# Kernel optimization log

Measured on AMD Instinct MI355X. Metric: run time of the kernel, lower is better.

## Reference

```python
import jax, jax.numpy as jnp
import numpy as np

B, T, I = 64, 1024, 256
H1, H2, O = 512, 512, 128


def setup_inputs() -> dict:
    key = jax.random.key(0)
    ks = jax.random.split(key, 4)
    x = jax.random.normal(ks[0], (B, T, I), dtype=jnp.float32)
    W1 = jax.random.normal(ks[1], (H1, I), dtype=jnp.float32) / np.sqrt(I).astype(np.float32)
    b1 = jnp.zeros((H1,), jnp.float32)
    tau_m1 = jnp.full((H1,), 2.0, jnp.float32)
    tau_n1 = jnp.full((H1,), 2.0, jnp.float32)
    W2 = jax.random.normal(ks[2], (H2, H1), dtype=jnp.float32) / np.sqrt(H1).astype(np.float32)
    b2 = jnp.zeros((H2,), jnp.float32)
    tau_m2 = jnp.full((H2,), 2.0, jnp.float32)
    tau_n2 = jnp.full((H2,), 2.0, jnp.float32)
    Wo = jax.random.normal(ks[3], (O, H2), dtype=jnp.float32) / np.sqrt(H2).astype(np.float32)
    bo = jnp.zeros((O,), jnp.float32)
    return {"x": x, "W1": W1, "b1": b1, "tau_m1": tau_m1, "tau_n1": tau_n1,
            "W2": W2, "b2": b2, "tau_m2": tau_m2, "tau_n2": tau_n2,
            "Wo": Wo, "bo": bo}


def reference(x, W1, b1, tau_m1, tau_n1, W2, b2, tau_m2, tau_n2, Wo, bo):
    dt = x.dtype
    beta1 = jax.nn.sigmoid(tau_n1)   # input-decay layer 1
    alpha1 = jax.nn.sigmoid(tau_m1)  # membrane-decay layer 1
    beta2 = jax.nn.sigmoid(tau_n2)
    alpha2 = jax.nn.sigmoid(tau_m2)

    # layer-1 dense projection is time-independent of state -> batch it: [T,B,H1]
    d_in1_all = jnp.swapaxes(jnp.einsum('bti,hi->bth', x, W1) + b1, 0, 1)

    def step(carry, d_in1):
        mem1, d1, mem2, d2 = carry
        # layer 1: dual-decay LIF
        d1 = beta1 * d1 + (1.0 - beta1) * d_in1
        mem1 = alpha1 * mem1 + (1.0 - alpha1) * d1
        s1 = (mem1 > 1.0).astype(dt)
        mem1 = mem1 * (1.0 - s1)
        # layer 2
        d_in2 = s1 @ W2.T + b2
        d2 = beta2 * d2 + (1.0 - beta2) * d_in2
        mem2 = alpha2 * mem2 + (1.0 - alpha2) * d2
        s2 = (mem2 > 1.0).astype(dt)
        mem2 = mem2 * (1.0 - s2)
        out = jax.nn.sigmoid(s2 @ Wo.T + bo)
        return (mem1, d1, mem2, d2), out

    init = (jnp.zeros((B, H1), dt), jnp.zeros((B, H1), dt),
            jnp.zeros((B, H2), dt), jnp.zeros((B, H2), dt))
    _, outs = jax.lax.scan(step, init, d_in1_all)  # [T,B,O]
    return jnp.swapaxes(outs, 0, 1)  # [B,T,O]
```

## Files before the change

### kernel.cpp

```cpp
#include <hip/hip_runtime.h>
#include <hip/hip_bf16.h>
#include <cstdint>

#define B_  64
#define T_  1024
#define I_  256
#define H1_ 512
#define H2_ 512
#define O_  128
#define CH_ 16
#define LL_ 64
#define GUARD_ 1e-3f

typedef unsigned long long u64;
typedef __attribute__((ext_vector_type(8))) short s8v;
typedef __attribute__((ext_vector_type(4))) float f4v;

__device__ __forceinline__ unsigned short f2bf(float f) {
    unsigned int u = __float_as_uint(f);
    unsigned int r = (u + 0x7FFFu + ((u >> 16) & 1u)) >> 16;
    return (unsigned short)r;
}

__global__ __launch_bounds__(256) void prep_kernel(
    const float* __restrict__ W2, const float* __restrict__ Wo,
    const float* __restrict__ W1,
    float* __restrict__ W2T, float* __restrict__ WoT,
    unsigned short* __restrict__ W1b,
    u64* __restrict__ zbuf, int nwords)
{
    int idx = blockIdx.x * 256 + threadIdx.x;
    if (idx < H1_ * H2_) {
        int h1 = idx / H2_, h2 = idx % H2_;
        W2T[idx] = W2[h2 * H1_ + h1];
    }
    if (idx < H2_ * O_) {
        int h2 = idx / O_, o = idx % O_;
        WoT[idx] = Wo[o * H2_ + h2];
    }
    if (idx < H1_ * I_) {
        W1b[idx] = f2bf(W1[idx]);
    }
    for (int i = idx; i < nwords; i += 256 * 1024)
        zbuf[i] = 0ull;
}

__global__ __launch_bounds__(1024, 1) void fused1_kernel(
    const float* __restrict__ X,
    const unsigned short* __restrict__ W1b,
    const float* __restrict__ b1,
    const float* __restrict__ tau_m1, const float* __restrict__ tau_n1,
    u64* __restrict__ s1_bits, u64* __restrict__ s1_any)
{
    __shared__ float rbuf[CH_][64][16];
    __shared__ float vd[CH_][64];
    __shared__ float meS[CH_][64];
    __shared__ float thS[CH_][64];
    __shared__ float memio[64];
    __shared__ int hdirty[64];
    __shared__ int anyd;

    const int tid = threadIdx.x;
    const int h  = tid & 63;
    const int c  = tid >> 6;
    const int id = blockIdx.x;
    const int b  = id & 63;
    const int hg = id >> 6;
    const int n0 = hg * 64;
    const int lr = tid & 15;
    const int lq = (tid >> 4) & 3;

    if (tid < 64) hdirty[tid] = 0;
    if (tid == 0) anyd = 0;

    f4v acc[4][4] = {};
    const float* xb = X + ((size_t)b * T_ + c * LL_) * I_;
    #pragma unroll
    for (int ks = 0; ks < 8; ks++) {
        s8v bf[4];
        #pragma unroll
        for (int ni = 0; ni < 4; ni++)
            bf[ni] = *reinterpret_cast<const s8v*>(
                W1b + (size_t)(n0 + ni * 16 + lr) * I_ + ks * 32 + lq * 8);
        #pragma unroll
        for (int mi = 0; mi < 4; mi++) {
            const float* xp = xb + (size_t)(mi * 16 + lr) * I_ + ks * 32 + lq * 8;
            float4 v0 = *reinterpret_cast<const float4*>(xp);
            float4 v1 = *reinterpret_cast<const float4*>(xp + 4);
            s8v a;
            a[0] = (short)((__float_as_uint(v0.x) + 0x8000u) >> 16);
            a[1] = (short)((__float_as_uint(v0.y) + 0x8000u) >> 16);
            a[2] = (short)((__float_as_uint(v0.z) + 0x8000u) >> 16);
            a[3] = (short)((__float_as_uint(v0.w) + 0x8000u) >> 16);
            a[4] = (short)((__float_as_uint(v1.x) + 0x8000u) >> 16);
            a[5] = (short)((__float_as_uint(v1.y) + 0x8000u) >> 16);
            a[6] = (short)((__float_as_uint(v1.z) + 0x8000u) >> 16);
            a[7] = (short)((__float_as_uint(v1.w) + 0x8000u) >> 16);
            #pragma unroll
            for (int ni = 0; ni < 4; ni++)
                acc[mi][ni] = __builtin_amdgcn_mfma_f32_16x16x32_bf16(
                    a, bf[ni], acc[mi][ni], 0, 0, 0);
        }
    }

    const float biasv = b1[n0 + h];
    const int swz_w = (lr & 3) ^ (lr >> 2);
    const int swz_r = (h & 3) ^ ((h >> 2) & 3);
    float arr[LL_];
    #pragma unroll
    for (int mi = 0; mi < 4; mi++) {
        #pragma unroll
        for (int ni = 0; ni < 4; ni++) {
            *reinterpret_cast<float4*>(&rbuf[c][ni * 16 + lr][(lq ^ swz_w) * 4]) =
                make_float4(acc[mi][ni][0], acc[mi][ni][1],
                            acc[mi][ni][2], acc[mi][ni][3]);
        }
        __builtin_amdgcn_wave_barrier();
        #pragma unroll
        for (int jq = 0; jq < 4; jq++) {
            float4 rv = *reinterpret_cast<const float4*>(&rbuf[c][h][(jq ^ swz_r) * 4]);
            arr[mi * 16 + jq * 4 + 0] = rv.x + biasv;
            arr[mi * 16 + jq * 4 + 1] = rv.y + biasv;
            arr[mi * 16 + jq * 4 + 2] = rv.z + biasv;
            arr[mi * 16 + jq * 4 + 3] = rv.w + biasv;
        }
        __builtin_amdgcn_wave_barrier();
    }

    const int hglob = n0 + h;
    float beta    = 1.f / (1.f + __expf(-tau_n1[hglob]));
    float alpha   = 1.f / (1.f + __expf(-tau_m1[hglob]));
    float ombeta  = 1.f - beta;
    float omalpha = 1.f - alpha;
    float bL = beta;  { bL *= bL; bL *= bL; bL *= bL; bL *= bL; bL *= bL; bL *= bL; }
    float aL = alpha; { aL *= aL; aL *= aL; aL *= aL; aL *= aL; aL *= aL; aL *= aL; }
    float ai = 1.0f / alpha;

    float d1 = 0.f;
    #pragma unroll
    for (int i = 0; i < LL_; i++) {
        d1 = fmaf(beta, d1, ombeta * arr[i]);
        arr[i] = d1;
    }
    vd[c][h] = d1;
    __syncthreads();

    float ds = 0.f;
    for (int cc = 0; cc < c; cc++) ds = fmaf(bL, ds, vd[cc][h]);

    float pc = ds, m = 0.f, api = 1.f, th = 3.4e38f;
    #pragma unroll
    for (int i = 0; i < LL_; i++) {
        pc *= beta;
        float dt = arr[i] + pc;
        arr[i] = dt;
        m = fmaf(alpha, m, omalpha * dt);
        api *= ai;
        th = fminf(th, (1.f - m) * api);
    }
    meS[c][h] = m;
    thS[c][h] = th;
    __syncthreads();

    float v = 0.f; bool dirty = false;
    for (int cc = 0; cc < c; cc++) {
        if (v > thS[cc][h] - GUARD_) dirty = true;
        v = fmaf(aL, v, meS[cc][h]);
    }
    if (v > th - GUARD_) dirty = true;
    if (dirty) { hdirty[h] = 1; atomicOr(&anyd, 1); }
    __syncthreads();

    if (anyd) {
        for (int cc = 0; cc < CH_; cc++) {
            if (c == cc && hdirty[h]) {
                float mi_ = (cc == 0) ? 0.f : memio[h];
                float mo;
                if (mi_ > th - GUARD_) {
                    float mem = mi_;
                    #pragma unroll
                    for (int i = 0; i < LL_; i++) {
                        mem = fmaf(alpha, mem, omalpha * arr[i]);
                        if (mem > 1.f) {
                            atomicOr(&s1_bits[((size_t)b * T_ + cc * LL_ + i) * 8 + hg], 1ull << h);
                            atomicOr(&s1_any[b * 16 + cc], 1ull << i);
                            mem = 0.f;
                        }
                    }
                    mo = mem;
                } else {
                    mo = fmaf(aL, mi_, m);
                }
                memio[h] = mo;
            }
            __syncthreads();
        }
    }
}

__device__ __noinline__ float gather_w2(const u64* __restrict__ w,
                                        const float* __restrict__ W2T, int hglob)
{
    float acc = 0.f;
    for (int q = 0; q < 8; q++) {
        u64 mq = w[q];
        while (mq) {
            int h1 = __ffsll((long long)mq) - 1;
            mq &= mq - 1;
            acc += W2T[(size_t)(q * 64 + h1) * H2_ + hglob];
        }
    }
    return acc;
}

__global__ __launch_bounds__(1024) void scan2_kernel(
    const float* __restrict__ W2T, const float* __restrict__ b2,
    const float* __restrict__ tau_m2, const float* __restrict__ tau_n2,
    const u64* __restrict__ s1_bits, const u64* __restrict__ s1_any,
    u64* __restrict__ s2_bits, u64* __restrict__ s2_any)
{
    __shared__ float vd[CH_][64];
    __shared__ float meS[CH_][64];
    __shared__ float thS[CH_][64];
    __shared__ float memio[64];
    __shared__ int hdirty[64];
    __shared__ int anyd;

    int tid = threadIdx.x;
    int h = tid & 63, c = tid >> 6;
    int id = blockIdx.x;
    int b  = id & 63;
    int hg = id >> 6;
    int hglob = hg * 64 + h;

    if (tid < 64) hdirty[tid] = 0;
    if (tid == 0) anyd = 0;

    float beta    = 1.f / (1.f + __expf(-tau_n2[hglob]));
    float alpha   = 1.f / (1.f + __expf(-tau_m2[hglob]));
    float ombeta  = 1.f - beta;
    float omalpha = 1.f - alpha;
    float bias    = b2[hglob];
    float bL = beta;  { bL *= bL; bL *= bL; bL *= bL; bL *= bL; bL *= bL; bL *= bL; }
    float aL = alpha; { aL *= aL; aL *= aL; aL *= aL; aL *= aL; aL *= aL; aL *= aL; }
    float ai = 1.0f / alpha;

    float arr[LL_];
    u64 aw = s1_any[b * 16 + c];
    float d2 = 0.f;
    if (aw == 0) {
        #pragma unroll
        for (int i = 0; i < LL_; i++) {
            d2 = fmaf(beta, d2, ombeta * bias);
            arr[i] = d2;
        }
    } else {
        #pragma unroll
        for (int i = 0; i < LL_; i++) {
            float dv = bias;
            if ((aw >> i) & 1ull)
                dv += gather_w2(s1_bits + ((size_t)b * T_ + c * LL_ + i) * 8, W2T, hglob);
            d2 = fmaf(beta, d2, ombeta * dv);
            arr[i] = d2;
        }
    }
    vd[c][h] = d2;
    __syncthreads();

    float ds = 0.f;
    for (int cc = 0; cc < c; cc++) ds = fmaf(bL, ds, vd[cc][h]);

    float pc = ds, m = 0.f, api = 1.f, th = 3.4e38f;
    #pragma unroll
    for (int i = 0; i < LL_; i++) {
        pc *= beta;
        float dt = arr[i] + pc;
        arr[i] = dt;
        m = fmaf(alpha, m, omalpha * dt);
        api *= ai;
        th = fminf(th, (1.f - m) * api);
    }
    meS[c][h] = m;
    thS[c][h] = th;
    __syncthreads();

    float v = 0.f; bool dirty = false;
    for (int cc = 0; cc < c; cc++) {
        if (v > thS[cc][h] - GUARD_) dirty = true;
        v = fmaf(aL, v, meS[cc][h]);
    }
    if (v > th - GUARD_) dirty = true;
    if (dirty) { hdirty[h] = 1; atomicOr(&anyd, 1); }
    __syncthreads();

    if (anyd) {
        for (int cc = 0; cc < CH_; cc++) {
            if (c == cc && hdirty[h]) {
                float mi_ = (cc == 0) ? 0.f : memio[h];
                float mo;
                if (mi_ > th - GUARD_) {
                    float mem = mi_;
                    #pragma unroll
                    for (int i = 0; i < LL_; i++) {
                        mem = fmaf(alpha, mem, omalpha * arr[i]);
                        if (mem > 1.f) {
                            atomicOr(&s2_bits[((size_t)b * T_ + cc * LL_ + i) * 8 + hg], 1ull << h);
                            atomicOr(&s2_any[b * 16 + cc], 1ull << i);
                            mem = 0.f;
                        }
                    }
                    mo = mem;
                } else {
                    mo = fmaf(aL, mi_, m);
                }
                memio[h] = mo;
            }
            __syncthreads();
        }
    }
}

__global__ __launch_bounds__(256) void out_kernel(
    const float* __restrict__ WoT, const float* __restrict__ bo,
    const u64* __restrict__ s2_bits, const u64* __restrict__ s2_any,
    float* __restrict__ out)
{
    int idx = blockIdx.x * 256 + threadIdx.x;
    int o4 = idx & 31;
    int t  = (idx >> 5) & 1023;
    int b  = idx >> 15;

    float4 z = *reinterpret_cast<const float4*>(bo + o4 * 4);
    if ((s2_any[b * 16 + (t >> 6)] >> (t & 63)) & 1ull) {
        const u64* w = s2_bits + ((size_t)b * T_ + t) * 8;
        for (int q = 0; q < 8; q++) {
            u64 mq = w[q];
            while (mq) {
                int h2 = __ffsll((long long)mq) - 1;
                mq &= mq - 1;
                float4 wv = *reinterpret_cast<const float4*>(
                    WoT + (size_t)(q * 64 + h2) * O_ + o4 * 4);
                z.x += wv.x; z.y += wv.y; z.z += wv.z; z.w += wv.w;
            }
        }
    }
    float4 r;
    r.x = 1.f / (1.f + __expf(-z.x));
    r.y = 1.f / (1.f + __expf(-z.y));
    r.z = 1.f / (1.f + __expf(-z.z));
    r.w = 1.f / (1.f + __expf(-z.w));
    *reinterpret_cast<float4*>(out + ((size_t)b * T_ + t) * O_ + o4 * 4) = r;
}

extern "C" void kernel_launch(void* const* d_in, const int* in_sizes, int n_in,
                              void* d_out, int out_size, void* d_ws, size_t ws_size,
                              hipStream_t stream)
{
    const float* x      = (const float*)d_in[0];
    const float* W1     = (const float*)d_in[1];
    const float* b1     = (const float*)d_in[2];
    const float* tau_m1 = (const float*)d_in[3];
    const float* tau_n1 = (const float*)d_in[4];
    const float* W2     = (const float*)d_in[5];
    const float* b2     = (const float*)d_in[6];
    const float* tau_m2 = (const float*)d_in[7];
    const float* tau_n2 = (const float*)d_in[8];
    const float* Wo     = (const float*)d_in[9];
    const float* bo     = (const float*)d_in[10];
    float* out = (float*)d_out;

    char* ws = (char*)d_ws;
    size_t off = 0;
    float* W2T = (float*)(ws + off);            off += (size_t)H1_ * H2_ * 4;
    float* WoT = (float*)(ws + off);            off += (size_t)H2_ * O_ * 4;
    unsigned short* W1b = (unsigned short*)(ws + off); off += (size_t)H1_ * I_ * 2;
    size_t zero_begin = off;
    u64* s1_any  = (u64*)(ws + off); off += (size_t)B_ * 16 * 8;
    u64* s2_any  = (u64*)(ws + off); off += (size_t)B_ * 16 * 8;
    u64* s1_bits = (u64*)(ws + off); off += (size_t)B_ * T_ * 8 * 8;
    u64* s2_bits = (u64*)(ws + off); off += (size_t)B_ * T_ * 8 * 8;
    int zero_words = (int)((off - zero_begin) / 8);

    prep_kernel<<<dim3(1024), dim3(256), 0, stream>>>(
        W2, Wo, W1, W2T, WoT, W1b, (u64*)(ws + zero_begin), zero_words);

    fused1_kernel<<<dim3(512), dim3(1024), 0, stream>>>(
        x, W1b, b1, tau_m1, tau_n1, s1_bits, s1_any);

    scan2_kernel<<<dim3(512), dim3(1024), 0, stream>>>(
        W2T, b2, tau_m2, tau_n2, s1_bits, s1_any, s2_bits, s2_any);

    out_kernel<<<dim3(B_ * 128), dim3(256), 0, stream>>>(
        WoT, bo, s2_bits, s2_any, out);
}
```

Measured before the change: 232.5 us.

## Pre-convert X to bf16 in a separate pass and stage W1 tile in LDS

Adds a conversion kernel that turns the fp32 input X into a bf16 copy in workspace. The fused layer-1 kernel then loads bf16 activations directly instead of fp32 data followed by in-register conversion. Each of the 8 hidden-group blocks per batch rereads X, so halving those bytes is meant to cut memory traffic. The per-block W1 tile is also loaded once into a swizzled LDS buffer rather than fetched from global memory per k-step. The cost is an extra full pass over X (read fp32, write bf16), 32 KB more shared memory per block, and a 32 MB workspace buffer.

```diff
diff --git a/kernel.cpp b/kernel.cpp
--- a/kernel.cpp
+++ b/kernel.cpp
@@ -15,11 +15,28 @@
 typedef unsigned long long u64;
 typedef __attribute__((ext_vector_type(8))) short s8v;
 typedef __attribute__((ext_vector_type(4))) float f4v;
+typedef __attribute__((ext_vector_type(8))) unsigned short us8v;
 
 __device__ __forceinline__ unsigned short f2bf(float f) {
     unsigned int u = __float_as_uint(f);
-    unsigned int r = (u + 0x7FFFu + ((u >> 16) & 1u)) >> 16;
-    return (unsigned short)r;
+    return (unsigned short)((u + 0x7FFFu + ((u >> 16) & 1u)) >> 16);
+}
+__device__ __forceinline__ unsigned short f2bf_rhu(float f) {
+    return (unsigned short)((__float_as_uint(f) + 0x8000u) >> 16);
+}
+
+__global__ __launch_bounds__(256) void xcvt_kernel(
+    const float* __restrict__ X, unsigned short* __restrict__ Xb)
+{
+    size_t i = ((size_t)blockIdx.x * 256 + threadIdx.x) * 8;
+    float4 v0 = *reinterpret_cast<const float4*>(X + i);
+    float4 v1 = *reinterpret_cast<const float4*>(X + i + 4);
+    us8v r;
+    r[0] = f2bf_rhu(v0.x); r[1] = f2bf_rhu(v0.y);
+    r[2] = f2bf_rhu(v0.z); r[3] = f2bf_rhu(v0.w);
+    r[4] = f2bf_rhu(v1.x); r[5] = f2bf_rhu(v1.y);
+    r[6] = f2bf_rhu(v1.z); r[7] = f2bf_rhu(v1.w);
+    *reinterpret_cast<us8v*>(Xb + i) = r;
 }
 
 __global__ __launch_bounds__(256) void prep_kernel(
@@ -46,12 +63,13 @@
 }
 
 __global__ __launch_bounds__(1024, 1) void fused1_kernel(
-    const float* __restrict__ X,
+    const unsigned short* __restrict__ Xb,
     const unsigned short* __restrict__ W1b,
     const float* __restrict__ b1,
     const float* __restrict__ tau_m1, const float* __restrict__ tau_n1,
     u64* __restrict__ s1_bits, u64* __restrict__ s1_any)
 {
+    __shared__ unsigned short w1s[64 * 256];
     __shared__ float rbuf[CH_][64][16];
     __shared__ float vd[CH_][64];
     __shared__ float meS[CH_][64];
@@ -73,34 +91,38 @@
     if (tid < 64) hdirty[tid] = 0;
     if (tid == 0) anyd = 0;
 
+    {
+        int row = tid >> 4, c2 = tid & 15;
+        const s8v* gsrc = reinterpret_cast<const s8v*>(
+            W1b + (size_t)(n0 + row) * I_ + c2 * 16);
+        int sw = row & 7;
+        s8v v0 = gsrc[0], v1 = gsrc[1];
+        *reinterpret_cast<s8v*>(&w1s[row * 256 + (((c2 * 2) ^ sw) << 3)])     = v0;
+        *reinterpret_cast<s8v*>(&w1s[row * 256 + (((c2 * 2 + 1) ^ sw) << 3)]) = v1;
+    }
+    __syncthreads();
+
     f4v acc[4][4] = {};
-    const float* xb = X + ((size_t)b * T_ + c * LL_) * I_;
+    const unsigned short* xb = Xb + ((size_t)b * T_ + c * LL_) * I_;
+    const int swb = lr & 7;
     #pragma unroll
     for (int ks = 0; ks < 8; ks++) {
+        s8v av[4];
+        #pragma unroll
+        for (int mi = 0; mi < 4; mi++)
+            av[mi] = *reinterpret_cast<const s8v*>(
+                xb + (size_t)(mi * 16 + lr) * I_ + ks * 32 + lq * 8);
         s8v bf[4];
         #pragma unroll
         for (int ni = 0; ni < 4; ni++)
             bf[ni] = *reinterpret_cast<const s8v*>(
-                W1b + (size_t)(n0 + ni * 16 + lr) * I_ + ks * 32 + lq * 8);
-        #pragma unroll
-        for (int mi = 0; mi < 4; mi++) {
-            const float* xp = xb + (size_t)(mi * 16 + lr) * I_ + ks * 32 + lq * 8;
-            float4 v0 = *reinterpret_cast<const float4*>(xp);
-            float4 v1 = *reinterpret_cast<const float4*>(xp + 4);
-            s8v a;
-            a[0] = (short)((__float_as_uint(v0.x) + 0x8000u) >> 16);
-            a[1] = (short)((__float_as_uint(v0.y) + 0x8000u) >> 16);
-            a[2] = (short)((__float_as_uint(v0.z) + 0x8000u) >> 16);
-            a[3] = (short)((__float_as_uint(v0.w) + 0x8000u) >> 16);
-            a[4] = (short)((__float_as_uint(v1.x) + 0x8000u) >> 16);
-            a[5] = (short)((__float_as_uint(v1.y) + 0x8000u) >> 16);
-            a[6] = (short)((__float_as_uint(v1.z) + 0x8000u) >> 16);
-            a[7] = (short)((__float_as_uint(v1.w) + 0x8000u) >> 16);
+                &w1s[(ni * 16 + lr) * 256 + ((((ks * 4) + lq) ^ swb) << 3)]);
+        #pragma unroll
+        for (int mi = 0; mi < 4; mi++)
             #pragma unroll
             for (int ni = 0; ni < 4; ni++)
                 acc[mi][ni] = __builtin_amdgcn_mfma_f32_16x16x32_bf16(
-                    a, bf[ni], acc[mi][ni], 0, 0, 0);
-        }
+                    av[mi], bf[ni], acc[mi][ni], 0, 0, 0);
     }
 
     const float biasv = b1[n0 + h];
@@ -374,6 +396,7 @@
     float* W2T = (float*)(ws + off);            off += (size_t)H1_ * H2_ * 4;
     float* WoT = (float*)(ws + off);            off += (size_t)H2_ * O_ * 4;
     unsigned short* W1b = (unsigned short*)(ws + off); off += (size_t)H1_ * I_ * 2;
+    unsigned short* Xb  = (unsigned short*)(ws + off); off += (size_t)B_ * T_ * I_ * 2;
     size_t zero_begin = off;
     u64* s1_any  = (u64*)(ws + off); off += (size_t)B_ * 16 * 8;
     u64* s2_any  = (u64*)(ws + off); off += (size_t)B_ * 16 * 8;
@@ -381,11 +404,13 @@
     u64* s2_bits = (u64*)(ws + off); off += (size_t)B_ * T_ * 8 * 8;
     int zero_words = (int)((off - zero_begin) / 8);
 
+    xcvt_kernel<<<dim3((B_ * T_ * I_) / (256 * 8)), dim3(256), 0, stream>>>(x, Xb);
+
     prep_kernel<<<dim3(1024), dim3(256), 0, stream>>>(
         W2, Wo, W1, W2T, WoT, W1b, (u64*)(ws + zero_begin), zero_words);
 
     fused1_kernel<<<dim3(512), dim3(1024), 0, stream>>>(
-        x, W1b, b1, tau_m1, tau_n1, s1_bits, s1_any);
+        Xb, W1b, b1, tau_m1, tau_n1, s1_bits, s1_any);
 
     scan2_kernel<<<dim3(512), dim3(1024), 0, stream>>>(
         W2T, b2, tau_m2, tau_n2, s1_bits, s1_any, s2_bits, s2_any);
```

After: 190.6 us. -18.0%, faster.
